# Kernel optimization log

Measured on AMD Instinct MI355X. Metric: run time of the kernel, lower is better.

Reference implementation:

```python
import jax, jax.numpy as jnp
import numpy as np

H, C = 8, 32          # heads, out_channels per head (H*C = 256)
D = H * C
NEG_SLOPE = 0.2
SELF_LOOP_TYPE = 6    # num_edge_types - 1
EPS_LN = 1e-5
EPS_BN = 1e-5


def _gat_layer(x, src, dst, ea, et, Ws, Wd, a_s, a_d, We, ae, te, Wo, bo, b, lg, lb):
    N = x.shape[0]
    xs = (x @ Ws).reshape(N, H, C)   # lin_src -> x_j features
    xd = (x @ Wd).reshape(N, H, C)   # lin_dst -> x_i features
    # per-node attention logits (gathered per edge): alpha = <x_i, att_src> + <x_j, att_dst>
    a_i = jnp.einsum('nhc,hc->nh', xd, a_s)  # paired with x_i (dst)
    a_j = jnp.einsum('nhc,hc->nh', xs, a_d)  # paired with x_j (src)
    alpha = a_i[dst] + a_j[src]                                  # [E, H]
    ef = (ea @ We).reshape(-1, H, C)                              # lin_edge
    alpha = alpha + jnp.einsum('ehc,hc->eh', ef, ae)
    tf = te[et].reshape(-1, H, C)                                 # edge_type_emb
    alpha = alpha + jnp.einsum('ehc,hc->eh', tf, ae)
    alpha = jnp.where(alpha >= 0, alpha, NEG_SLOPE * alpha)       # leaky_relu
    # segment softmax over destination nodes (every node has a self loop)
    m = jax.ops.segment_max(alpha, dst, num_segments=N)
    e = jnp.exp(alpha - m[dst])
    s = jax.ops.segment_sum(e, dst, num_segments=N)
    alpha = e / (s[dst] + 1e-16)                                  # [E, H]
    # dropout is identity in eval mode
    msg = xs[src] * alpha[:, :, None]                             # [E, H, C]
    out = jax.ops.segment_sum(msg, dst, num_segments=N).reshape(N, D)
    out = out @ Wo + bo + b                                       # lin_out + bias
    mu = out.mean(-1, keepdims=True)
    var = out.var(-1, keepdims=True)
    out = (out - mu) / jnp.sqrt(var + EPS_LN) * lg + lb           # layer norm
    return out + x                                                # in_channels == H*C residual


def _bn_relu(x, g, bvec, relu=True):
    mu = x.mean(0)
    var = x.var(0)
    x = (x - mu) / jnp.sqrt(var + EPS_BN) * g + bvec
    return jnp.maximum(x, 0.0) if relu else x


def _forward(x, edge_index, edge_attr, edge_types,
             Ws1, Wd1, as1, ad1, We1, ae1, te1, Wo1, bo1, b1, lg1, lb1,
             Ws2, Wd2, as2, ad2, We2, ae2, te2, Wo2, bo2, b2, lg2, lb2,
             bng1, bnb1, bng2, bnb2):
    N = x.shape[0]
    loops = jnp.arange(N, dtype=edge_index.dtype)
    src = jnp.concatenate([edge_index[0], loops])
    dst = jnp.concatenate([edge_index[1], loops])
    ea = jnp.concatenate([edge_attr, jnp.ones((N, edge_attr.shape[1]), edge_attr.dtype)])
    et = jnp.concatenate([edge_types, jnp.full((N,), SELF_LOOP_TYPE, edge_types.dtype)])
    residual = x  # in_channels == out_channels -> identity projection
    out = _gat_layer(x, src, dst, ea, et, Ws1, Wd1, as1, ad1, We1, ae1, te1, Wo1, bo1, b1, lg1, lb1)
    out = _bn_relu(out, bng1, bnb1, relu=True)   # dropout identity in eval
    out = _gat_layer(out, src, dst, ea, et, Ws2, Wd2, as2, ad2, We2, ae2, te2, Wo2, bo2, b2, lg2, lb2)
    out = _bn_relu(out, bng2, bnb2, relu=False)
    return jnp.maximum(out + residual, 0.0)


def setup_inputs() -> dict:
    key = jax.random.key(0)
    ks = jax.random.split(key, 32)
    N, E, EDIM, NTYPES = 20000, 320000, 16, 7
    d = {}
    d['x'] = jax.random.normal(ks[0], (N, D), jnp.float32)
    d['edge_index'] = jax.random.randint(ks[1], (2, E), 0, N, jnp.int64)
    d['edge_attr'] = jax.random.normal(ks[2], (E, EDIM), jnp.float32)
    d['edge_types'] = jax.random.randint(ks[3], (E,), 0, NTYPES, jnp.int64)
    def glorot(k, shape):
        fan = shape[-2] + shape[-1] if len(shape) >= 2 else shape[-1] + 1
        return jax.random.uniform(k, shape, jnp.float32, -1.0, 1.0) * np.sqrt(6.0 / fan)
    i = 4
    for L in ('1', '2'):
        d['Ws' + L] = glorot(ks[i], (D, D)); i += 1
        d['Wd' + L] = glorot(ks[i], (D, D)); i += 1
        d['as' + L] = glorot(ks[i], (H, C)); i += 1
        d['ad' + L] = glorot(ks[i], (H, C)); i += 1
        d['We' + L] = glorot(ks[i], (EDIM, D)); i += 1
        d['ae' + L] = glorot(ks[i], (H, C)); i += 1
        d['te' + L] = glorot(ks[i], (NTYPES, D)); i += 1
        d['Wo' + L] = glorot(ks[i], (D, D)); i += 1
        d['bo' + L] = jnp.zeros((D,), jnp.float32)
        d['b' + L] = jnp.zeros((D,), jnp.float32)
        d['lg' + L] = jnp.ones((D,), jnp.float32)
        d['lb' + L] = jnp.zeros((D,), jnp.float32)
    d['bng1'] = jnp.ones((D,), jnp.float32); d['bnb1'] = jnp.zeros((D,), jnp.float32)
    d['bng2'] = jnp.ones((D,), jnp.float32); d['bnb2'] = jnp.zeros((D,), jnp.float32)
    return d


def reference(x, edge_index, edge_attr, edge_types,
              Ws1, Wd1, as1, ad1, We1, ae1, te1, Wo1, bo1, b1, lg1, lb1,
              Ws2, Wd2, as2, ad2, We2, ae2, te2, Wo2, bo2, b2, lg2, lb2,
              bng1, bnb1, bng2, bnb2):
    return _forward(x, edge_index, edge_attr, edge_types,
                    Ws1, Wd1, as1, ad1, We1, ae1, te1, Wo1, bo1, b1, lg1, lb1,
                    Ws2, Wd2, as2, ad2, We2, ae2, te2, Wo2, bo2, b2, lg2, lb2,
                    bng1, bnb1, bng2, bnb2)
```

## Files before the change

kernel.cpp:

```cpp
#include <hip/hip_runtime.h>

#define DD 256
#define HH 8
#define CC 32

typedef __attribute__((ext_vector_type(8))) short short8;
typedef __attribute__((ext_vector_type(4))) float f32x4;

static __device__ __forceinline__ unsigned short f2b(float f){
  unsigned u = __float_as_uint(f);
  u = u + 0x7FFFu + ((u >> 16) & 1u);
  return (unsigned short)(u >> 16);
}
static __device__ __forceinline__ float b2f(unsigned short s){
  return __uint_as_float(((unsigned)s) << 16);
}

__global__ void k_zero_i(int* p, int n){ int i=blockIdx.x*blockDim.x+threadIdx.x; if(i<n) p[i]=0; }

__global__ void k_count(const int* __restrict__ dstE, int E, int N, int* cnt){
  int e=blockIdx.x*blockDim.x+threadIdx.x;
  if(e<E+N){ int d=(e<E)? dstE[e] : (e-E); atomicAdd(&cnt[d],1); }
}

__global__ __launch_bounds__(1024) void k_scan(const int* __restrict__ cnt, int N, int* row_off, int* cursor){
  __shared__ int part[1024];
  int t=threadIdx.x;
  int chunk=(N+1023)>>10;
  int s=0;
  for(int j=0;j<chunk;j++){ int i=t*chunk+j; if(i<N) s+=cnt[i]; }
  part[t]=s; __syncthreads();
  for(int off=1; off<1024; off<<=1){
    int v=(t>=off)? part[t-off]:0;
    __syncthreads();
    part[t]+=v;
    __syncthreads();
  }
  int run=(t==0)?0:part[t-1];
  for(int j=0;j<chunk;j++){ int i=t*chunk+j; if(i<N){ row_off[i]=run; cursor[i]=run; run+=cnt[i]; } }
  if(t==1023) row_off[N]=part[1023];
}

__global__ void k_fill(const int* __restrict__ srcE, const int* __restrict__ dstE, int E, int N,
                       int* cursor, int* epos, int* esrc){
  int e=blockIdx.x*blockDim.x+threadIdx.x;
  if(e>=E+N) return;
  int s,d;
  if(e<E){ s=srcE[e]; d=dstE[e]; } else { s=e-E; d=s; }
  int pos=atomicAdd(&cursor[d],1);
  epos[e]=pos; esrc[pos]=s;
}

__global__ void k_cvt_wT4(const float* __restrict__ W0, const float* __restrict__ W1,
                          const float* __restrict__ W2, const float* __restrict__ W3,
                          unsigned short* __restrict__ T0, unsigned short* __restrict__ T1,
                          unsigned short* __restrict__ T2, unsigned short* __restrict__ T3){
  int m=blockIdx.y, c=blockIdx.x, k=threadIdx.x;
  const float* W = (m==0)?W0:(m==1)?W1:(m==2)?W2:W3;
  unsigned short* T = (m==0)?T0:(m==1)?T1:(m==2)?T2:T3;
  T[(size_t)c*DD+k] = f2b(W[(size_t)k*DD+c]);
}

__global__ void k_pre2(const float* __restrict__ Wd1, const float* __restrict__ as1,
                       const float* __restrict__ We1, const float* __restrict__ ae1,
                       const float* __restrict__ te1,
                       const float* __restrict__ Wd2, const float* __restrict__ as2,
                       const float* __restrict__ We2, const float* __restrict__ ae2,
                       const float* __restrict__ te2,
                       float* wd_as1, float* v_e1, float* t_a1,
                       float* wd_as2, float* v_e2, float* t_a2){
  int L=blockIdx.x;
  const float* Wd=L?Wd2:Wd1; const float* as_=L?as2:as1;
  const float* We=L?We2:We1; const float* ae=L?ae2:ae1; const float* te=L?te2:te1;
  float* wd_as=L?wd_as2:wd_as1; float* v_e=L?v_e2:v_e1; float* t_a=L?t_a2:t_a1;
  int t=threadIdx.x;
  for(int idx=t; idx<DD*HH; idx+=256){
    int k=idx>>3, h=idx&7;
    const float* w=&Wd[k*DD+h*CC]; const float* a=&as_[h*CC];
    float s=0;
    #pragma unroll
    for(int c=0;c<CC;c++) s+=w[c]*a[c];
    wd_as[idx]=s;
  }
  for(int idx=t; idx<16*HH; idx+=256){
    int k=idx>>3, h=idx&7;
    const float* w=&We[k*DD+h*CC]; const float* a=&ae[h*CC];
    float s=0;
    #pragma unroll
    for(int c=0;c<CC;c++) s+=w[c]*a[c];
    v_e[idx]=s;
  }
  for(int idx=t; idx<7*HH; idx+=256){
    int k=idx>>3, h=idx&7;
    const float* w=&te[k*DD+h*CC]; const float* a=&ae[h*CC];
    float s=0;
    #pragma unroll
    for(int c=0;c<CC;c++) s+=w[c]*a[c];
    t_a[idx]=s;
  }
}

__global__ __launch_bounds__(256) void k_cvt_x(const float* __restrict__ xin, const float* __restrict__ wd_as,
                        unsigned short* __restrict__ xb, float* __restrict__ a_i, int N){
  __shared__ float red[DD*HH];
  __shared__ float part[8][8];
  int n=blockIdx.x, tid=threadIdx.x;
  float v=xin[(size_t)n*DD+tid];
  xb[(size_t)n*DD+tid]=f2b(v);
  #pragma unroll
  for(int h=0;h<HH;h++) red[tid*HH+h]=v*wd_as[tid*HH+h];
  __syncthreads();
  if(tid<64){
    int h=tid&7, ch=tid>>3;
    float s=0.f;
    for(int k=ch*32;k<ch*32+32;k++) s+=red[k*HH+h];
    part[ch][h]=s;
  }
  __syncthreads();
  if(tid<8){
    float s=0.f;
    #pragma unroll
    for(int ch=0;ch<8;ch++) s+=part[ch][tid];
    a_i[(size_t)n*HH+tid]=s;
  }
}

template<bool OUTBF16, bool BIAS, bool AJ>
__global__ __launch_bounds__(256) void k_gemm_mfma(const unsigned short* __restrict__ A,
                                                   const unsigned short* __restrict__ Bt,
                                                   const float* __restrict__ bia1, const float* __restrict__ bia2,
                                                   const float* __restrict__ ad, float* __restrict__ a_j,
                                                   void* __restrict__ Cout, int N){
  __shared__ char lds[4096 + 8192];
  int tid=threadIdx.x;
  int w=tid>>6, l=tid&63;
  int row0=blockIdx.y*64, col0=blockIdx.x*128;

  int sr=tid>>2, skc=tid&3;
  int kcs=skc^((sr>>1)&3);
  int aslot=sr*4+skc;
  int bslot1=sr*4+skc, bslot2=(sr+64)*4+skc;
  int gr=row0+sr;
  size_t boff1=(size_t)(col0+sr)*DD, boff2=(size_t)(col0+64+sr)*DD;

  int x15=l&15;
  int lp=x15*64 + ((l>>4)^((x15>>1)&3))*16;

  f32x4 acc[4][2];
  #pragma unroll
  for(int i=0;i<4;i++){ acc[i][0]=(f32x4)0.f; acc[i][1]=(f32x4)0.f; }

  const short8 zero8=(short8)0;
  short8 av,bv1,bv2;
  av  = (gr<N) ? *(const short8*)&A[(size_t)gr*DD + kcs*8] : zero8;
  bv1 = *(const short8*)&Bt[boff1 + kcs*8];
  bv2 = *(const short8*)&Bt[boff2 + kcs*8];

  for(int kt=0;kt<DD;kt+=32){
    __syncthreads();
    *(short8*)(lds + aslot*16) = av;
    *(short8*)(lds + 4096 + bslot1*16) = bv1;
    *(short8*)(lds + 4096 + bslot2*16) = bv2;
    __syncthreads();
    if(kt+32<DD){
      int ko=kt+32+kcs*8;
      av  = (gr<N) ? *(const short8*)&A[(size_t)gr*DD + ko] : zero8;
      bv1 = *(const short8*)&Bt[boff1 + ko];
      bv2 = *(const short8*)&Bt[boff2 + ko];
    }
    short8 af[4], bf[2];
    #pragma unroll
    for(int mf=0;mf<4;mf++) af[mf]=*(short8*)(lds + mf*1024 + lp);
    #pragma unroll
    for(int nf=0;nf<2;nf++) bf[nf]=*(short8*)(lds + 4096 + (32*w+16*nf)*64 + lp);
    #pragma unroll
    for(int mf=0;mf<4;mf++)
      #pragma unroll
      for(int nf=0;nf<2;nf++)
        acc[mf][nf]=__builtin_amdgcn_mfma_f32_16x16x32_bf16(af[mf],bf[nf],acc[mf][nf],0,0,0);
  }

  int lcol=x15, lrow4=(l>>4)*4;
  float ad0=0.f, ad1=0.f;
  if(AJ){ ad0=ad[col0+32*w+lcol]; ad1=ad[col0+32*w+16+lcol]; }
  int head=(col0>>5)+w;
  #pragma unroll
  for(int mf=0;mf<4;mf++){
    #pragma unroll
    for(int nf=0;nf<2;nf++){
      int col=col0 + 32*w + 16*nf + lcol;
      float badd = BIAS ? (bia1[col]+bia2[col]) : 0.f;
      #pragma unroll
      for(int rr=0;rr<4;rr++){
        int row=row0 + 16*mf + lrow4 + rr;
        if(row<N){
          float v=acc[mf][nf][rr]+badd;
          if(OUTBF16) ((unsigned short*)Cout)[(size_t)row*DD+col]=f2b(v);
          else        ((float*)Cout)[(size_t)row*DD+col]=v;
        }
      }
    }
    if(AJ){
      #pragma unroll
      for(int rr=0;rr<4;rr++){
        float t=acc[mf][0][rr]*ad0 + acc[mf][1][rr]*ad1;
        t+=__shfl_xor(t,1); t+=__shfl_xor(t,2);
        t+=__shfl_xor(t,4); t+=__shfl_xor(t,8);
        int row=row0 + 16*mf + lrow4 + rr;
        if(x15==0 && row<N) a_j[(size_t)row*HH+head]=t;
      }
    }
  }
}

__global__ void k_edge(const int* __restrict__ srcE, const int* __restrict__ dstE,
                       const float* __restrict__ ea, const int* __restrict__ et,
                       const int* __restrict__ epos,
                       const float* __restrict__ a_i, const float* __restrict__ a_j,
                       const float* __restrict__ v_e, const float* __restrict__ t_a,
                       float* __restrict__ alphaP, int E, int N){
  int e=blockIdx.x*blockDim.x+threadIdx.x;
  if(e>=E+N) return;
  int s,d,ty;
  float eattr[16];
  if(e<E){
    s=srcE[e]; d=dstE[e]; ty=et[e];
    float4 q0=*(const float4*)&ea[(size_t)e*16+0];
    float4 q1=*(const float4*)&ea[(size_t)e*16+4];
    float4 q2=*(const float4*)&ea[(size_t)e*16+8];
    float4 q3=*(const float4*)&ea[(size_t)e*16+12];
    eattr[0]=q0.x;eattr[1]=q0.y;eattr[2]=q0.z;eattr[3]=q0.w;
    eattr[4]=q1.x;eattr[5]=q1.y;eattr[6]=q1.z;eattr[7]=q1.w;
    eattr[8]=q2.x;eattr[9]=q2.y;eattr[10]=q2.z;eattr[11]=q2.w;
    eattr[12]=q3.x;eattr[13]=q3.y;eattr[14]=q3.z;eattr[15]=q3.w;
  }else{
    s=e-E; d=s; ty=6;
    #pragma unroll
    for(int k=0;k<16;k++) eattr[k]=1.f;
  }
  int pos=epos[e];
  const float* ai=&a_i[(size_t)d*8];
  const float* aj=&a_j[(size_t)s*8];
  #pragma unroll
  for(int h=0;h<8;h++){
    float v=ai[h]+aj[h]+t_a[ty*8+h];
    #pragma unroll
    for(int k=0;k<16;k++) v+=eattr[k]*v_e[k*8+h];
    alphaP[(size_t)pos*8+h] = (v>=0.f)? v : 0.2f*v;
  }
}

__global__ __launch_bounds__(256) void k_agg(const int* __restrict__ row_off,
                      const int* __restrict__ esrc, const float* __restrict__ alphaP,
                      const unsigned short* __restrict__ ysb, unsigned short* __restrict__ aggb, int N){
  int wv=threadIdx.x>>6, l=threadIdx.x&63;
  int n=blockIdx.x*4+wv;
  if(n>=N) return;
  int beg=row_off[n], deg=row_off[n+1]-beg;
  int slotL=l>>3, headL=l&7;
  float mx=-3e38f;
  for(int i=slotL;i<deg;i+=8) mx=fmaxf(mx, alphaP[(size_t)(beg+i)*8+headL]);
  mx=fmaxf(mx,__shfl_xor(mx,8));
  mx=fmaxf(mx,__shfl_xor(mx,16));
  mx=fmaxf(mx,__shfl_xor(mx,32));
  int ghead=l>>3;
  float ssum=0.f, acc0=0.f, acc1=0.f, acc2=0.f, acc3=0.f;
  float a_c; int s_c;
  {
    int i=slotL; bool ok=(i<deg); int ic=ok?i:(deg-1);
    a_c = ok ? alphaP[(size_t)(beg+i)*8+headL] : -3e38f;
    s_c = esrc[beg+ic];
  }
  for(int base=0;base<deg;base+=8){
    float a_n=-3e38f; int s_n=0;
    if(base+8<deg){
      int i=base+8+slotL; bool ok=(i<deg); int ic=ok?i:(deg-1);
      a_n = ok ? alphaP[(size_t)(beg+i)*8+headL] : -3e38f;
      s_n = esrc[beg+ic];
    }
    float wvv=__expf(a_c-mx);
    int cnt=min(8,deg-base);
    #pragma unroll
    for(int u=0;u<8;u++){
      if(u<cnt){
        float wgt=__shfl(wvv,(u<<3)|ghead);
        int   si =__shfl(s_c,(u<<3));
        ssum+=wgt;
        ushort4 y=*(const ushort4*)&ysb[(size_t)si*DD+4*l];
        acc0+=wgt*b2f(y.x); acc1+=wgt*b2f(y.y); acc2+=wgt*b2f(y.z); acc3+=wgt*b2f(y.w);
      }
    }
    a_c=a_n; s_c=s_n;
  }
  float inv=1.f/(ssum+1e-16f);
  ushort4 o;
  o.x=f2b(acc0*inv); o.y=f2b(acc1*inv); o.z=f2b(acc2*inv); o.w=f2b(acc3*inv);
  *(ushort4*)&aggb[(size_t)n*DD+4*l]=o;
}

#define NB_LN 512
__global__ __launch_bounds__(256) void k_lnbn(const float* __restrict__ z, const float* __restrict__ xin,
                         const float* __restrict__ lg, const float* __restrict__ lb,
                         float* __restrict__ hout, float* __restrict__ psum, float* __restrict__ psq, int N){
  __shared__ float sps[4][DD], spq[4][DD];
  int b=blockIdx.x, tid=threadIdx.x, wv=tid>>6, l=tid&63;
  int c0=4*l;
  float4 lgv=*(const float4*)&lg[c0];
  float4 lbv=*(const float4*)&lb[c0];
  float ps0=0.f,ps1=0.f,ps2=0.f,ps3=0.f,pq0=0.f,pq1=0.f,pq2=0.f,pq3=0.f;
  for(int r=b*4+wv; r<N; r+=NB_LN*4){
    float4 v=*(const float4*)&z[(size_t)r*DD+c0];
    float s=v.x+v.y+v.z+v.w;
    float q=v.x*v.x+v.y*v.y+v.z*v.z+v.w*v.w;
    #pragma unroll
    for(int off=1;off<64;off<<=1){ s+=__shfl_xor(s,off); q+=__shfl_xor(q,off); }
    float mu=s*(1.f/DD);
    float var=q*(1.f/DD)-mu*mu;
    float rstd=rsqrtf(var+1e-5f);
    float4 xr=*(const float4*)&xin[(size_t)r*DD+c0];
    float4 h;
    h.x=(v.x-mu)*rstd*lgv.x+lbv.x+xr.x;
    h.y=(v.y-mu)*rstd*lgv.y+lbv.y+xr.y;
    h.z=(v.z-mu)*rstd*lgv.z+lbv.z+xr.z;
    h.w=(v.w-mu)*rstd*lgv.w+lbv.w+xr.w;
    *(float4*)&hout[(size_t)r*DD+c0]=h;
    ps0+=h.x;ps1+=h.y;ps2+=h.z;ps3+=h.w;
    pq0+=h.x*h.x;pq1+=h.y*h.y;pq2+=h.z*h.z;pq3+=h.w*h.w;
  }
  sps[wv][c0+0]=ps0; sps[wv][c0+1]=ps1; sps[wv][c0+2]=ps2; sps[wv][c0+3]=ps3;
  spq[wv][c0+0]=pq0; spq[wv][c0+1]=pq1; spq[wv][c0+2]=pq2; spq[wv][c0+3]=pq3;
  __syncthreads();
  float s=sps[0][tid]+sps[1][tid]+sps[2][tid]+sps[3][tid];
  float q=spq[0][tid]+spq[1][tid]+spq[2][tid]+spq[3][tid];
  psum[(size_t)b*DD+tid]=s;
  psq[(size_t)b*DD+tid]=q;
}

__global__ __launch_bounds__(256) void k_bnfin(const float* __restrict__ psum, const float* __restrict__ psq,
                        const float* __restrict__ g, const float* __restrict__ b,
                        float* scale, float* shift, int N){
  __shared__ float rs[256], rq[256];
  int c=blockIdx.x, tid=threadIdx.x;
  rs[tid]=psum[(size_t)tid*DD+c]+psum[(size_t)(tid+256)*DD+c];
  rq[tid]=psq[(size_t)tid*DD+c]+psq[(size_t)(tid+256)*DD+c];
  __syncthreads();
  #pragma unroll
  for(int off=128;off>0;off>>=1){
    if(tid<off){ rs[tid]+=rs[tid+off]; rq[tid]+=rq[tid+off]; }
    __syncthreads();
  }
  if(tid==0){
    float inv=1.f/(float)N;
    float mu=rs[0]*inv;
    float var=rq[0]*inv - mu*mu;
    float sc=g[c]*rsqrtf(var+1e-5f);
    scale[c]=sc;
    shift[c]=b[c]-mu*sc;
  }
}

#define NB_BA 1024
template<bool RES, bool CVT>
__global__ __launch_bounds__(256) void k_bnapply(const float* __restrict__ hm, const float* __restrict__ scale,
                          const float* __restrict__ shift, const float* __restrict__ res,
                          float* __restrict__ outp, unsigned short* __restrict__ xb,
                          const float* __restrict__ wd_as, float* __restrict__ a_i, int N){
  int b=blockIdx.x, tid=threadIdx.x, wv=tid>>6, l=tid&63;
  int c0=4*l;
  float4 sc=*(const float4*)&scale[c0];
  float4 sh=*(const float4*)&shift[c0];
  float wa[4][8];
  if(CVT){
    #pragma unroll
    for(int j=0;j<4;j++)
      #pragma unroll
      for(int h=0;h<8;h++) wa[j][h]=wd_as[(c0+j)*8+h];
  }
  for(int n=b*4+wv; n<N; n+=NB_BA*4){
    float4 v=*(const float4*)&hm[(size_t)n*DD+c0];
    v.x=v.x*sc.x+sh.x; v.y=v.y*sc.y+sh.y; v.z=v.z*sc.z+sh.z; v.w=v.w*sc.w+sh.w;
    if(RES){
      float4 rr=*(const float4*)&res[(size_t)n*DD+c0];
      v.x+=rr.x; v.y+=rr.y; v.z+=rr.z; v.w+=rr.w;
    }
    v.x=fmaxf(v.x,0.f); v.y=fmaxf(v.y,0.f); v.z=fmaxf(v.z,0.f); v.w=fmaxf(v.w,0.f);
    *(float4*)&outp[(size_t)n*DD+c0]=v;
    if(CVT){
      ushort4 xo; xo.x=f2b(v.x); xo.y=f2b(v.y); xo.z=f2b(v.z); xo.w=f2b(v.w);
      *(ushort4*)&xb[(size_t)n*DD+c0]=xo;
      float ai[8];
      #pragma unroll
      for(int h=0;h<8;h++) ai[h]=v.x*wa[0][h]+v.y*wa[1][h]+v.z*wa[2][h]+v.w*wa[3][h];
      #pragma unroll
      for(int off=1;off<64;off<<=1){
        #pragma unroll
        for(int h=0;h<8;h++) ai[h]+=__shfl_xor(ai[h],off);
      }
      if(l==0){
        float4 A; A.x=ai[0];A.y=ai[1];A.z=ai[2];A.w=ai[3];
        float4 B; B.x=ai[4];B.y=ai[5];B.z=ai[6];B.w=ai[7];
        *(float4*)&a_i[(size_t)n*HH]=A;
        *(float4*)&a_i[(size_t)n*HH+4]=B;
      }
    }
  }
}

extern "C" void kernel_launch(void* const* d_in, const int* in_sizes, int n_in,
                              void* d_out, int out_size, void* d_ws, size_t ws_size,
                              hipStream_t stream) {
  const float* x  = (const float*)d_in[0];
  const int*   ei = (const int*)d_in[1];
  const float* ea = (const float*)d_in[2];
  const int*   et = (const int*)d_in[3];
  int N = in_sizes[0]/DD;
  int E = in_sizes[3];
  int Etot = E+N;
  const int* srcE = ei;
  const int* dstE = ei + E;

  const float* Ws1=(const float*)d_in[4];  const float* Wd1=(const float*)d_in[5];
  const float* as1=(const float*)d_in[6];  const float* ad1=(const float*)d_in[7];
  const float* We1=(const float*)d_in[8];  const float* ae1=(const float*)d_in[9];
  const float* te1=(const float*)d_in[10]; const float* Wo1=(const float*)d_in[11];
  const float* bo1=(const float*)d_in[12]; const float* b1 =(const float*)d_in[13];
  const float* lg1=(const float*)d_in[14]; const float* lb1=(const float*)d_in[15];
  const float* Ws2=(const float*)d_in[16]; const float* Wd2=(const float*)d_in[17];
  const float* as2=(const float*)d_in[18]; const float* ad2=(const float*)d_in[19];
  const float* We2=(const float*)d_in[20]; const float* ae2=(const float*)d_in[21];
  const float* te2=(const float*)d_in[22]; const float* Wo2=(const float*)d_in[23];
  const float* bo2=(const float*)d_in[24]; const float* b2 =(const float*)d_in[25];
  const float* lg2=(const float*)d_in[26]; const float* lb2=(const float*)d_in[27];
  const float* bng1=(const float*)d_in[28]; const float* bnb1=(const float*)d_in[29];
  const float* bng2=(const float*)d_in[30]; const float* bnb2=(const float*)d_in[31];

  char* p=(char*)d_ws;
  auto alloc=[&](size_t bytes)->void*{ void* r=(void*)p; p+=(bytes+255)&~(size_t)255; return r; };
  unsigned short* xb   =(unsigned short*)alloc((size_t)N*DD*2);
  unsigned short* ysb  =(unsigned short*)alloc((size_t)N*DD*2);
  unsigned short* aggb =(unsigned short*)alloc((size_t)N*DD*2);
  float* Sreg  =(float*)alloc((size_t)N*DD*4);
  float* xout1 =(float*)alloc((size_t)N*DD*4);
  float* a_i   =(float*)alloc((size_t)N*HH*4);
  float* a_j   =(float*)alloc((size_t)N*HH*4);
  float* wd_as1=(float*)alloc(DD*HH*4);
  float* v_e1  =(float*)alloc(16*HH*4);
  float* t_a1  =(float*)alloc(7*HH*4);
  float* wd_as2=(float*)alloc(DD*HH*4);
  float* v_e2  =(float*)alloc(16*HH*4);
  float* t_a2  =(float*)alloc(7*HH*4);
  float* psum  =(float*)alloc((size_t)NB_LN*DD*4);
  float* psq   =(float*)alloc((size_t)NB_LN*DD*4);
  float* scl   =(float*)alloc(256*4);
  float* shf   =(float*)alloc(256*4);
  unsigned short* Wsb1T=(unsigned short*)alloc((size_t)DD*DD*2);
  unsigned short* Wob1T=(unsigned short*)alloc((size_t)DD*DD*2);
  unsigned short* Wsb2T=(unsigned short*)alloc((size_t)DD*DD*2);
  unsigned short* Wob2T=(unsigned short*)alloc((size_t)DD*DD*2);
  int* cnt     =(int*)alloc((size_t)N*4);
  int* row_off =(int*)alloc((size_t)(N+1)*4);
  int* cursor  =(int*)alloc((size_t)N*4);
  int* epos    =(int*)alloc((size_t)Etot*4);
  int* esrc    =(int*)alloc((size_t)Etot*4);
  float* hbuf  =(float*)d_out;
  float* alphaP=Sreg;
  float* zbuf=Sreg;

  dim3 gg(2,(N+63)/64);
  int aggGrid=(N+3)/4;

  k_zero_i<<<(N+255)/256,256,0,stream>>>(cnt,N);
  k_count<<<(Etot+255)/256,256,0,stream>>>(dstE,E,N,cnt);
  k_scan<<<1,1024,0,stream>>>(cnt,N,row_off,cursor);
  k_fill<<<(Etot+255)/256,256,0,stream>>>(srcE,dstE,E,N,cursor,epos,esrc);
  k_cvt_wT4<<<dim3(DD,4),DD,0,stream>>>(Ws1,Wo1,Ws2,Wo2,Wsb1T,Wob1T,Wsb2T,Wob2T);
  k_pre2<<<2,256,0,stream>>>(Wd1,as1,We1,ae1,te1,Wd2,as2,We2,ae2,te2,
                             wd_as1,v_e1,t_a1,wd_as2,v_e2,t_a2);

  k_cvt_x<<<N,256,0,stream>>>(x,wd_as1,xb,a_i,N);
  k_gemm_mfma<true,false,true><<<gg,256,0,stream>>>(xb,Wsb1T,nullptr,nullptr,ad1,a_j,(void*)ysb,N);
  k_edge<<<(Etot+255)/256,256,0,stream>>>(srcE,dstE,ea,et,epos,a_i,a_j,v_e1,t_a1,alphaP,E,N);
  k_agg<<<aggGrid,256,0,stream>>>(row_off,esrc,alphaP,ysb,aggb,N);
  k_gemm_mfma<false,true,false><<<gg,256,0,stream>>>(aggb,Wob1T,bo1,b1,nullptr,nullptr,(void*)zbuf,N);
  k_lnbn<<<NB_LN,256,0,stream>>>(zbuf,x,lg1,lb1,hbuf,psum,psq,N);
  k_bnfin<<<DD,256,0,stream>>>(psum,psq,bng1,bnb1,scl,shf,N);
  k_bnapply<false,true><<<NB_BA,256,0,stream>>>(hbuf,scl,shf,nullptr,xout1,xb,wd_as2,a_i,N);

  k_gemm_mfma<true,false,true><<<gg,256,0,stream>>>(xb,Wsb2T,nullptr,nullptr,ad2,a_j,(void*)ysb,N);
  k_edge<<<(Etot+255)/256,256,0,stream>>>(srcE,dstE,ea,et,epos,a_i,a_j,v_e2,t_a2,alphaP,E,N);
  k_agg<<<aggGrid,256,0,stream>>>(row_off,esrc,alphaP,ysb,aggb,N);
  k_gemm_mfma<false,true,false><<<gg,256,0,stream>>>(aggb,Wob2T,bo2,b2,nullptr,nullptr,(void*)zbuf,N);
  k_lnbn<<<NB_LN,256,0,stream>>>(zbuf,xout1,lg2,lb2,hbuf,psum,psq,N);
  k_bnfin<<<DD,256,0,stream>>>(psum,psq,bng2,bnb2,scl,shf,N);
  k_bnapply<true,false><<<NB_BA,256,0,stream>>>(hbuf,scl,shf,x,(float*)d_out,nullptr,nullptr,nullptr,N);
}
```

Baseline: 321.6 us.

## Fuse output GEMM with LayerNorm and BN partial sums; grid-stride x conversion

The second per-layer GEMM now computes a full 64x256 row tile per block, so it can apply bias, LayerNorm and the residual add and emit per-column BatchNorm partial sums directly. This drops the fp32 z buffer round trip and the separate LN kernel. The per-node x conversion kernel is rewritten as a grid-stride, wave-per-row kernel that reduces with shuffles instead of one block per node using LDS. The trade-off is a wider GEMM tile with more accumulators and fewer blocks, plus a larger partial-sum array that the bnfin kernel must loop over.

```diff
diff --git a/kernel.cpp b/kernel.cpp
--- a/kernel.cpp
+++ b/kernel.cpp
@@ -100,37 +100,42 @@
   }
 }
 
-__global__ __launch_bounds__(256) void k_cvt_x(const float* __restrict__ xin, const float* __restrict__ wd_as,
-                        unsigned short* __restrict__ xb, float* __restrict__ a_i, int N){
-  __shared__ float red[DD*HH];
-  __shared__ float part[8][8];
-  int n=blockIdx.x, tid=threadIdx.x;
-  float v=xin[(size_t)n*DD+tid];
-  xb[(size_t)n*DD+tid]=f2b(v);
-  #pragma unroll
-  for(int h=0;h<HH;h++) red[tid*HH+h]=v*wd_as[tid*HH+h];
-  __syncthreads();
-  if(tid<64){
-    int h=tid&7, ch=tid>>3;
-    float s=0.f;
-    for(int k=ch*32;k<ch*32+32;k++) s+=red[k*HH+h];
-    part[ch][h]=s;
-  }
-  __syncthreads();
-  if(tid<8){
-    float s=0.f;
-    #pragma unroll
-    for(int ch=0;ch<8;ch++) s+=part[ch][tid];
-    a_i[(size_t)n*HH+tid]=s;
-  }
-}
-
-template<bool OUTBF16, bool BIAS, bool AJ>
-__global__ __launch_bounds__(256) void k_gemm_mfma(const unsigned short* __restrict__ A,
-                                                   const unsigned short* __restrict__ Bt,
-                                                   const float* __restrict__ bia1, const float* __restrict__ bia2,
-                                                   const float* __restrict__ ad, float* __restrict__ a_j,
-                                                   void* __restrict__ Cout, int N){
+#define NB_BA 1024
+__global__ __launch_bounds__(256) void k_cvt_x2(const float* __restrict__ xin, const float* __restrict__ wd_as,
+                         unsigned short* __restrict__ xb, float* __restrict__ a_i, int N){
+  int b=blockIdx.x, tid=threadIdx.x, wv=tid>>6, l=tid&63;
+  int c0=4*l;
+  float wa[4][8];
+  #pragma unroll
+  for(int j=0;j<4;j++)
+    #pragma unroll
+    for(int h=0;h<8;h++) wa[j][h]=wd_as[(c0+j)*8+h];
+  for(int n=b*4+wv; n<N; n+=NB_BA*4){
+    float4 v=*(const float4*)&xin[(size_t)n*DD+c0];
+    ushort4 xo; xo.x=f2b(v.x); xo.y=f2b(v.y); xo.z=f2b(v.z); xo.w=f2b(v.w);
+    *(ushort4*)&xb[(size_t)n*DD+c0]=xo;
+    float ai[8];
+    #pragma unroll
+    for(int h=0;h<8;h++) ai[h]=v.x*wa[0][h]+v.y*wa[1][h]+v.z*wa[2][h]+v.w*wa[3][h];
+    #pragma unroll
+    for(int off=1;off<64;off<<=1){
+      #pragma unroll
+      for(int h=0;h<8;h++) ai[h]+=__shfl_xor(ai[h],off);
+    }
+    if(l==0){
+      float4 A; A.x=ai[0];A.y=ai[1];A.z=ai[2];A.w=ai[3];
+      float4 B; B.x=ai[4];B.y=ai[5];B.z=ai[6];B.w=ai[7];
+      *(float4*)&a_i[(size_t)n*HH]=A;
+      *(float4*)&a_i[(size_t)n*HH+4]=B;
+    }
+  }
+}
+
+template<bool AJ>
+__global__ __launch_bounds__(256) void k_gemm1(const unsigned short* __restrict__ A,
+                                               const unsigned short* __restrict__ Bt,
+                                               const float* __restrict__ ad, float* __restrict__ a_j,
+                                               unsigned short* __restrict__ Cout, int N){
   __shared__ char lds[4096 + 8192];
   int tid=threadIdx.x;
   int w=tid>>6, l=tid&63;
@@ -189,15 +194,10 @@
     #pragma unroll
     for(int nf=0;nf<2;nf++){
       int col=col0 + 32*w + 16*nf + lcol;
-      float badd = BIAS ? (bia1[col]+bia2[col]) : 0.f;
       #pragma unroll
       for(int rr=0;rr<4;rr++){
         int row=row0 + 16*mf + lrow4 + rr;
-        if(row<N){
-          float v=acc[mf][nf][rr]+badd;
-          if(OUTBF16) ((unsigned short*)Cout)[(size_t)row*DD+col]=f2b(v);
-          else        ((float*)Cout)[(size_t)row*DD+col]=v;
-        }
+        if(row<N) Cout[(size_t)row*DD+col]=f2b(acc[mf][nf][rr]);
       }
     }
     if(AJ){
@@ -209,6 +209,151 @@
         int row=row0 + 16*mf + lrow4 + rr;
         if(x15==0 && row<N) a_j[(size_t)row*HH+head]=t;
       }
+    }
+  }
+}
+
+__global__ __launch_bounds__(256) void k_gemm_ln(const unsigned short* __restrict__ A,
+                                                 const unsigned short* __restrict__ Bt,
+                                                 const float* __restrict__ bo, const float* __restrict__ bvec,
+                                                 const float* __restrict__ xin,
+                                                 const float* __restrict__ lg, const float* __restrict__ lb,
+                                                 float* __restrict__ hout,
+                                                 float* __restrict__ psum, float* __restrict__ psq, int N){
+  __shared__ char lds[4096 + 16384];
+  int tid=threadIdx.x;
+  int w=tid>>6, l=tid&63;
+  int row0=blockIdx.x*64;
+
+  int sr=tid>>2, skc=tid&3;
+  int kcs=skc^((sr>>1)&3);
+  int aslot=tid;
+  int gr=row0+sr;
+  size_t boff0=(size_t)(sr)*DD, boff1=(size_t)(64+sr)*DD,
+         boff2=(size_t)(128+sr)*DD, boff3=(size_t)(192+sr)*DD;
+  int bs0=sr*4+skc, bs1=(sr+64)*4+skc, bs2=(sr+128)*4+skc, bs3=(sr+192)*4+skc;
+
+  int x15=l&15;
+  int lp=x15*64 + ((l>>4)^((x15>>1)&3))*16;
+
+  f32x4 acc[4][4];
+  #pragma unroll
+  for(int i=0;i<4;i++)
+    #pragma unroll
+    for(int j=0;j<4;j++) acc[i][j]=(f32x4)0.f;
+
+  const short8 zero8=(short8)0;
+  short8 av,b0,b1,b2,b3;
+  av = (gr<N) ? *(const short8*)&A[(size_t)gr*DD + kcs*8] : zero8;
+  b0=*(const short8*)&Bt[boff0 + kcs*8];
+  b1=*(const short8*)&Bt[boff1 + kcs*8];
+  b2=*(const short8*)&Bt[boff2 + kcs*8];
+  b3=*(const short8*)&Bt[boff3 + kcs*8];
+
+  for(int kt=0;kt<DD;kt+=32){
+    __syncthreads();
+    *(short8*)(lds + aslot*16) = av;
+    *(short8*)(lds + 4096 + bs0*16) = b0;
+    *(short8*)(lds + 4096 + bs1*16) = b1;
+    *(short8*)(lds + 4096 + bs2*16) = b2;
+    *(short8*)(lds + 4096 + bs3*16) = b3;
+    __syncthreads();
+    if(kt+32<DD){
+      int ko=kt+32+kcs*8;
+      av = (gr<N) ? *(const short8*)&A[(size_t)gr*DD + ko] : zero8;
+      b0=*(const short8*)&Bt[boff0 + ko];
+      b1=*(const short8*)&Bt[boff1 + ko];
+      b2=*(const short8*)&Bt[boff2 + ko];
+      b3=*(const short8*)&Bt[boff3 + ko];
+    }
+    short8 af[4], bf[4];
+    #pragma unroll
+    for(int mf=0;mf<4;mf++) af[mf]=*(short8*)(lds + mf*1024 + lp);
+    #pragma unroll
+    for(int nf=0;nf<4;nf++) bf[nf]=*(short8*)(lds + 4096 + w*4096 + nf*1024 + lp);
+    #pragma unroll
+    for(int mf=0;mf<4;mf++)
+      #pragma unroll
+      for(int nf=0;nf<4;nf++)
+        acc[mf][nf]=__builtin_amdgcn_mfma_f32_16x16x32_bf16(af[mf],bf[nf],acc[mf][nf],0,0,0);
+  }
+
+  int lrow4=(l>>4)*4;
+  float lgv[4], lbv[4];
+  #pragma unroll
+  for(int nf=0;nf<4;nf++){
+    int col=64*w+16*nf+x15;
+    float badd=bo[col]+bvec[col];
+    lgv[nf]=lg[col]; lbv[nf]=lb[col];
+    #pragma unroll
+    for(int mf=0;mf<4;mf++)
+      #pragma unroll
+      for(int rr=0;rr<4;rr++) acc[mf][nf][rr]+=badd;
+  }
+  __syncthreads();
+  float* rs   =(float*)lds;
+  float* rq   =(float*)(lds+1024);
+  float* mus  =(float*)(lds+2048);
+  float* rstds=(float*)(lds+2304);
+  #pragma unroll
+  for(int mf=0;mf<4;mf++){
+    #pragma unroll
+    for(int rr=0;rr<4;rr++){
+      float t=acc[mf][0][rr]+acc[mf][1][rr]+acc[mf][2][rr]+acc[mf][3][rr];
+      float q=acc[mf][0][rr]*acc[mf][0][rr]+acc[mf][1][rr]*acc[mf][1][rr]
+             +acc[mf][2][rr]*acc[mf][2][rr]+acc[mf][3][rr]*acc[mf][3][rr];
+      t+=__shfl_xor(t,1); q+=__shfl_xor(q,1);
+      t+=__shfl_xor(t,2); q+=__shfl_xor(q,2);
+      t+=__shfl_xor(t,4); q+=__shfl_xor(q,4);
+      t+=__shfl_xor(t,8); q+=__shfl_xor(q,8);
+      if(x15==0){
+        int row=16*mf+lrow4+rr;
+        rs[w*64+row]=t; rq[w*64+row]=q;
+      }
+    }
+  }
+  __syncthreads();
+  if(tid<64){
+    float S=rs[tid]+rs[64+tid]+rs[128+tid]+rs[192+tid];
+    float Q=rq[tid]+rq[64+tid]+rq[128+tid]+rq[192+tid];
+    float mu=S*(1.f/DD);
+    float var=Q*(1.f/DD)-mu*mu;
+    mus[tid]=mu;
+    rstds[tid]=rsqrtf(var+1e-5f);
+  }
+  __syncthreads();
+  float cps[4]={0.f,0.f,0.f,0.f}, cqs[4]={0.f,0.f,0.f,0.f};
+  #pragma unroll
+  for(int mf=0;mf<4;mf++){
+    #pragma unroll
+    for(int rr=0;rr<4;rr++){
+      int row=16*mf+lrow4+rr;
+      int grow=row0+row;
+      bool ok=(grow<N);
+      float mu=mus[row], rstd=rstds[row];
+      #pragma unroll
+      for(int nf=0;nf<4;nf++){
+        int col=64*w+16*nf+x15;
+        float h=0.f;
+        if(ok){
+          h=(acc[mf][nf][rr]-mu)*rstd*lgv[nf]+lbv[nf]+xin[(size_t)grow*DD+col];
+          hout[(size_t)grow*DD+col]=h;
+        }
+        cps[nf]+=h; cqs[nf]+=h*h;
+      }
+    }
+  }
+  #pragma unroll
+  for(int nf=0;nf<4;nf++){
+    cps[nf]+=__shfl_xor(cps[nf],16); cqs[nf]+=__shfl_xor(cqs[nf],16);
+    cps[nf]+=__shfl_xor(cps[nf],32); cqs[nf]+=__shfl_xor(cqs[nf],32);
+  }
+  if(l<16){
+    #pragma unroll
+    for(int nf=0;nf<4;nf++){
+      int col=64*w+16*nf+l;
+      psum[(size_t)blockIdx.x*DD+col]=cps[nf];
+      psq [(size_t)blockIdx.x*DD+col]=cqs[nf];
     }
   }
 }
@@ -298,51 +443,14 @@
   *(ushort4*)&aggb[(size_t)n*DD+4*l]=o;
 }
 
-#define NB_LN 512
-__global__ __launch_bounds__(256) void k_lnbn(const float* __restrict__ z, const float* __restrict__ xin,
-                         const float* __restrict__ lg, const float* __restrict__ lb,
-                         float* __restrict__ hout, float* __restrict__ psum, float* __restrict__ psq, int N){
-  __shared__ float sps[4][DD], spq[4][DD];
-  int b=blockIdx.x, tid=threadIdx.x, wv=tid>>6, l=tid&63;
-  int c0=4*l;
-  float4 lgv=*(const float4*)&lg[c0];
-  float4 lbv=*(const float4*)&lb[c0];
-  float ps0=0.f,ps1=0.f,ps2=0.f,ps3=0.f,pq0=0.f,pq1=0.f,pq2=0.f,pq3=0.f;
-  for(int r=b*4+wv; r<N; r+=NB_LN*4){
-    float4 v=*(const float4*)&z[(size_t)r*DD+c0];
-    float s=v.x+v.y+v.z+v.w;
-    float q=v.x*v.x+v.y*v.y+v.z*v.z+v.w*v.w;
-    #pragma unroll
-    for(int off=1;off<64;off<<=1){ s+=__shfl_xor(s,off); q+=__shfl_xor(q,off); }
-    float mu=s*(1.f/DD);
-    float var=q*(1.f/DD)-mu*mu;
-    float rstd=rsqrtf(var+1e-5f);
-    float4 xr=*(const float4*)&xin[(size_t)r*DD+c0];
-    float4 h;
-    h.x=(v.x-mu)*rstd*lgv.x+lbv.x+xr.x;
-    h.y=(v.y-mu)*rstd*lgv.y+lbv.y+xr.y;
-    h.z=(v.z-mu)*rstd*lgv.z+lbv.z+xr.z;
-    h.w=(v.w-mu)*rstd*lgv.w+lbv.w+xr.w;
-    *(float4*)&hout[(size_t)r*DD+c0]=h;
-    ps0+=h.x;ps1+=h.y;ps2+=h.z;ps3+=h.w;
-    pq0+=h.x*h.x;pq1+=h.y*h.y;pq2+=h.z*h.z;pq3+=h.w*h.w;
-  }
-  sps[wv][c0+0]=ps0; sps[wv][c0+1]=ps1; sps[wv][c0+2]=ps2; sps[wv][c0+3]=ps3;
-  spq[wv][c0+0]=pq0; spq[wv][c0+1]=pq1; spq[wv][c0+2]=pq2; spq[wv][c0+3]=pq3;
-  __syncthreads();
-  float s=sps[0][tid]+sps[1][tid]+sps[2][tid]+sps[3][tid];
-  float q=spq[0][tid]+spq[1][tid]+spq[2][tid]+spq[3][tid];
-  psum[(size_t)b*DD+tid]=s;
-  psq[(size_t)b*DD+tid]=q;
-}
-
 __global__ __launch_bounds__(256) void k_bnfin(const float* __restrict__ psum, const float* __restrict__ psq,
                         const float* __restrict__ g, const float* __restrict__ b,
-                        float* scale, float* shift, int N){
+                        float* scale, float* shift, int N, int nb){
   __shared__ float rs[256], rq[256];
   int c=blockIdx.x, tid=threadIdx.x;
-  rs[tid]=psum[(size_t)tid*DD+c]+psum[(size_t)(tid+256)*DD+c];
-  rq[tid]=psq[(size_t)tid*DD+c]+psq[(size_t)(tid+256)*DD+c];
+  float s=0.f,q=0.f;
+  for(int i=tid;i<nb;i+=256){ s+=psum[(size_t)i*DD+c]; q+=psq[(size_t)i*DD+c]; }
+  rs[tid]=s; rq[tid]=q;
   __syncthreads();
   #pragma unroll
   for(int off=128;off>0;off>>=1){
@@ -359,7 +467,6 @@
   }
 }
 
-#define NB_BA 1024
 template<bool RES, bool CVT>
 __global__ __launch_bounds__(256) void k_bnapply(const float* __restrict__ hm, const float* __restrict__ scale,
                           const float* __restrict__ shift, const float* __restrict__ res,
@@ -439,7 +546,7 @@
   unsigned short* xb   =(unsigned short*)alloc((size_t)N*DD*2);
   unsigned short* ysb  =(unsigned short*)alloc((size_t)N*DD*2);
   unsigned short* aggb =(unsigned short*)alloc((size_t)N*DD*2);
-  float* Sreg  =(float*)alloc((size_t)N*DD*4);
+  float* alphaP=(float*)alloc((size_t)Etot*HH*4);
   float* xout1 =(float*)alloc((size_t)N*DD*4);
   float* a_i   =(float*)alloc((size_t)N*HH*4);
   float* a_j   =(float*)alloc((size_t)N*HH*4);
@@ -449,8 +556,9 @@
   float* wd_as2=(float*)alloc(DD*HH*4);
   float* v_e2  =(float*)alloc(16*HH*4);
   float* t_a2  =(float*)alloc(7*HH*4);
-  float* psum  =(float*)alloc((size_t)NB_LN*DD*4);
-  float* psq   =(float*)alloc((size_t)NB_LN*DD*4);
+  int nbLN=(N+63)/64;
+  float* psum  =(float*)alloc((size_t)nbLN*DD*4);
+  float* psq   =(float*)alloc((size_t)nbLN*DD*4);
   float* scl   =(float*)alloc(256*4);
   float* shf   =(float*)alloc(256*4);
   unsigned short* Wsb1T=(unsigned short*)alloc((size_t)DD*DD*2);
@@ -463,8 +571,6 @@
   int* epos    =(int*)alloc((size_t)Etot*4);
   int* esrc    =(int*)alloc((size_t)Etot*4);
   float* hbuf  =(float*)d_out;
-  float* alphaP=Sreg;
-  float* zbuf=Sreg;
 
   dim3 gg(2,(N+63)/64);
   int aggGrid=(N+3)/4;
@@ -477,20 +583,18 @@
   k_pre2<<<2,256,0,stream>>>(Wd1,as1,We1,ae1,te1,Wd2,as2,We2,ae2,te2,
                              wd_as1,v_e1,t_a1,wd_as2,v_e2,t_a2);
 
-  k_cvt_x<<<N,256,0,stream>>>(x,wd_as1,xb,a_i,N);
-  k_gemm_mfma<true,false,true><<<gg,256,0,stream>>>(xb,Wsb1T,nullptr,nullptr,ad1,a_j,(void*)ysb,N);
+  k_cvt_x2<<<NB_BA,256,0,stream>>>(x,wd_as1,xb,a_i,N);
+  k_gemm1<true><<<gg,256,0,stream>>>(xb,Wsb1T,ad1,a_j,ysb,N);
   k_edge<<<(Etot+255)/256,256,0,stream>>>(srcE,dstE,ea,et,epos,a_i,a_j,v_e1,t_a1,alphaP,E,N);
   k_agg<<<aggGrid,256,0,stream>>>(row_off,esrc,alphaP,ysb,aggb,N);
-  k_gemm_mfma<false,true,false><<<gg,256,0,stream>>>(aggb,Wob1T,bo1,b1,nullptr,nullptr,(void*)zbuf,N);
-  k_lnbn<<<NB_LN,256,0,stream>>>(zbuf,x,lg1,lb1,hbuf,psum,psq,N);
-  k_bnfin<<<DD,256,0,stream>>>(psum,psq,bng1,bnb1,scl,shf,N);
+  k_gemm_ln<<<nbLN,256,0,stream>>>(aggb,Wob1T,bo1,b1,x,lg1,lb1,hbuf,psum,psq,N);
+  k_bnfin<<<DD,256,0,stream>>>(psum,psq,bng1,bnb1,scl,shf,N,nbLN);
   k_bnapply<false,true><<<NB_BA,256,0,stream>>>(hbuf,scl,shf,nullptr,xout1,xb,wd_as2,a_i,N);
 
-  k_gemm_mfma<true,false,true><<<gg,256,0,stream>>>(xb,Wsb2T,nullptr,nullptr,ad2,a_j,(void*)ysb,N);
+  k_gemm1<true><<<gg,256,0,stream>>>(xb,Wsb2T,ad2,a_j,ysb,N);
   k_edge<<<(Etot+255)/256,256,0,stream>>>(srcE,dstE,ea,et,epos,a_i,a_j,v_e2,t_a2,alphaP,E,N);
   k_agg<<<aggGrid,256,0,stream>>>(row_off,esrc,alphaP,ysb,aggb,N);
-  k_gemm_mfma<false,true,false><<<gg,256,0,stream>>>(aggb,Wob2T,bo2,b2,nullptr,nullptr,(void*)zbuf,N);
-  k_lnbn<<<NB_LN,256,0,stream>>>(zbuf,xout1,lg2,lb2,hbuf,psum,psq,N);
-  k_bnfin<<<DD,256,0,stream>>>(psum,psq,bng2,bnb2,scl,shf,N);
+  k_gemm_ln<<<nbLN,256,0,stream>>>(aggb,Wob2T,bo2,b2,xout1,lg2,lb2,hbuf,psum,psq,N);
+  k_bnfin<<<DD,256,0,stream>>>(psum,psq,bng2,bnb2,scl,shf,N,nbLN);
   k_bnapply<true,false><<<NB_BA,256,0,stream>>>(hbuf,scl,shf,x,(float*)d_out,nullptr,nullptr,nullptr,N);
 }
```

Result: slower. 335.9 us (+4.4%).
